# Kernel tuning notes

Measured on AMD Instinct MI355X. Metric: run time of the kernel, lower is better.

## Reference

```python
import jax, jax.numpy as jnp
import numpy as np

N_NODES = 20000
N_EDGES = 320000
D = 256          # out_channels (== in_channels here, so PyG zero-padding is a no-op)
NUM_LAYERS = 5


def setup_inputs() -> dict:
    key = jax.random.key(0)
    ks = jax.random.split(key, 8)
    x = jax.random.normal(ks[0], (N_NODES, D), dtype=jnp.float32)
    src = jax.random.randint(ks[1], (N_EDGES,), 0, N_NODES)
    dst = jax.random.randint(ks[2], (N_EDGES,), 0, N_NODES)
    edge_index = jnp.stack([src, dst]).astype(jnp.int64)
    edge_attr = jax.random.uniform(ks[3], (N_EDGES,), dtype=jnp.float32)
    s = 1.0 / np.sqrt(D)
    # per-layer message transform weights [L, D, D]
    weight = jax.random.uniform(ks[4], (NUM_LAYERS, D, D), minval=-s, maxval=s, dtype=jnp.float32)
    # GRUCell parameters (torch layout: [3*D, D] for W_ih/W_hh, [3*D] biases; gate order r, z, n)
    w_ih = jax.random.uniform(ks[5], (3 * D, D), minval=-s, maxval=s, dtype=jnp.float32)
    w_hh = jax.random.uniform(ks[6], (3 * D, D), minval=-s, maxval=s, dtype=jnp.float32)
    b = jax.random.uniform(ks[7], (2, 3 * D), minval=-s, maxval=s, dtype=jnp.float32)
    return {"x": x, "edge_index": edge_index, "edge_attr": edge_attr,
            "weight": weight, "w_ih": w_ih, "w_hh": w_hh,
            "b_ih": b[0], "b_hh": b[1]}


def gru_cell(m, h, w_ih, w_hh, b_ih, b_hh):
    gi = m @ w_ih.T + b_ih   # [N, 3D]
    gh = h @ w_hh.T + b_hh   # [N, 3D]
    i_r, i_z, i_n = jnp.split(gi, 3, axis=1)
    h_r, h_z, h_n = jnp.split(gh, 3, axis=1)
    r = jax.nn.sigmoid(i_r + h_r)
    z = jax.nn.sigmoid(i_z + h_z)
    n = jnp.tanh(i_n + r * h_n)
    return (1.0 - z) * n + z * h


def reference(x, edge_index, edge_attr, weight, w_ih, w_hh, b_ih, b_hh):
    src = edge_index[0]
    dst = edge_index[1]
    n_nodes = x.shape[0]
    h = x  # in_channels == out_channels, so no zero padding needed
    for i in range(weight.shape[0]):
        m = h @ weight[i]                                  # [N, D] transformed messages
        msgs = m[src] * edge_attr[:, None]                 # gather + edge weighting [E, D]
        agg = jax.ops.segment_sum(msgs, dst, num_segments=n_nodes)  # scatter-add [N, D]
        h = gru_cell(agg, h, w_ih, w_hh, b_ih, b_hh)
    return h
```

## Files before the change

### kernel.cpp

```cpp
#include <hip/hip_runtime.h>
#include <hip/hip_bf16.h>

#define NN 20000
#define NE 320000
#define DD 256

typedef __attribute__((ext_vector_type(8))) short bf16x8;
typedef __attribute__((ext_vector_type(4))) float f32x4;
typedef __attribute__((ext_vector_type(4))) int   int4v;
typedef __attribute__((ext_vector_type(4))) float float4v;

typedef __attribute__((address_space(1))) unsigned int gas_uint;
typedef __attribute__((address_space(3))) unsigned int las_uint;
static __device__ __forceinline__ void gload16(const void* g, void* l) {
    __builtin_amdgcn_global_load_lds((gas_uint*)g, (las_uint*)l, 16, 0, 0);
}

__device__ __forceinline__ unsigned short f2bf(float f) {
    union { float f; unsigned u; } v; v.f = f;
    unsigned r = v.u + 0x7fffu + ((v.u >> 16) & 1u);
    return (unsigned short)(r >> 16);
}
__device__ __forceinline__ float bf2f(unsigned short h) {
    union { unsigned u; float f; } v; v.u = ((unsigned)h) << 16;
    return v.f;
}
__device__ __forceinline__ float fast_sigmoid(float x) {
    return 1.f / (1.f + __expf(-x));
}
__device__ __forceinline__ float fast_tanh(float x) {
    x = fminf(fmaxf(x, -30.f), 30.f);
    float e = __expf(-2.f * x);
    return (1.f - e) / (1.f + e);
}


__global__ void cast_kernel(const float* __restrict__ in, unsigned short* __restrict__ out, int n) {
    int i = (blockIdx.x * blockDim.x + threadIdx.x) * 4;
    if (i >= n) return;
    float4v v = *reinterpret_cast<const float4v*>(in + i);
    uint2 o;
    o.x = (unsigned)f2bf(v.x) | ((unsigned)f2bf(v.y) << 16);
    o.y = (unsigned)f2bf(v.z) | ((unsigned)f2bf(v.w) << 16);
    *reinterpret_cast<uint2*>(out + i) = o;
}

__global__ __launch_bounds__(256) void pgemm_kernel(const unsigned short* __restrict__ A,
                                                    const unsigned short* __restrict__ Bt,
                                                    unsigned short* __restrict__ C) {
    __shared__ __align__(16) unsigned short As[128 * 64];
    __shared__ __align__(16) unsigned short Bs[64 * 64];
    const int t = threadIdx.x;
    const int lane = t & 63;
    const int w = t >> 6;
    const int wr = w >> 1, wc = w & 1;
    const int m0 = blockIdx.y * 128;
    const int n0 = blockIdx.x * 64;

    f32x4 acc[4][2];
    const f32x4 z4 = {0.f, 0.f, 0.f, 0.f};
    for (int i = 0; i < 4; ++i) for (int j = 0; j < 2; ++j) acc[i][j] = z4;

    for (int kt = 0; kt < 4; ++kt) {
        const int k0 = kt * 64;
#pragma unroll
        for (int rnd = 0; rnd < 4; ++rnd) {
            int cb = rnd * 256 + (w << 6);
            int c = cb + lane;
            int row = c >> 3, sl = c & 7;
            int gsl = sl ^ (row & 7);
            gload16(A + (size_t)(m0 + row) * 256 + k0 + gsl * 8, &As[cb * 8]);
        }
#pragma unroll
        for (int rnd = 0; rnd < 2; ++rnd) {
            int cb = rnd * 256 + (w << 6);
            int c = cb + lane;
            int row = c >> 3, sl = c & 7;
            int gsl = sl ^ (row & 7);
            gload16(Bt + (size_t)(n0 + row) * 256 + k0 + gsl * 8, &Bs[cb * 8]);
        }
        __syncthreads();
#pragma unroll
        for (int ks = 0; ks < 2; ++ks) {
            const int slot = ks * 4 + (lane >> 4);
            bf16x8 a[4], b[2];
#pragma unroll
            for (int mi = 0; mi < 4; ++mi) {
                int row = wr * 64 + mi * 16 + (lane & 15);
                a[mi] = *reinterpret_cast<const bf16x8*>(&As[row * 64 + ((slot ^ (row & 7)) << 3)]);
            }
#pragma unroll
            for (int ni = 0; ni < 2; ++ni) {
                int row = wc * 32 + ni * 16 + (lane & 15);
                b[ni] = *reinterpret_cast<const bf16x8*>(&Bs[row * 64 + ((slot ^ (row & 7)) << 3)]);
            }
#pragma unroll
            for (int mi = 0; mi < 4; ++mi)
#pragma unroll
                for (int ni = 0; ni < 2; ++ni)
                    acc[mi][ni] = __builtin_amdgcn_mfma_f32_16x16x32_bf16(a[mi], b[ni], acc[mi][ni], 0, 0, 0);
        }
        __syncthreads();
    }
#pragma unroll
    for (int mi = 0; mi < 4; ++mi)
#pragma unroll
        for (int ni = 0; ni < 2; ++ni)
#pragma unroll
            for (int r = 0; r < 4; ++r) {
                int grow = m0 + wr * 64 + mi * 16 + (lane >> 4) * 4 + r;
                int gcol = n0 + wc * 32 + ni * 16 + (lane & 15);
                C[(size_t)grow * 768 + gcol] = f2bf(acc[mi][ni][r]);
            }
}

__global__ void wc5_kernel(const unsigned short* __restrict__ Pall,
                           const float* __restrict__ whh,
                           unsigned short* __restrict__ Wc5) {
    int id = blockIdx.x * 256 + threadIdx.x;
    int k  = id & 255;
    int t2 = id >> 8;
    int n3 = t2 % 768;
    int t3 = t2 / 768;
    int hf = t3 & 1;
    int l  = t3 >> 1;
    int g3 = (n3 >> 4) % 3;
    int dg = n3 / 48;
    int dc = n3 & 15;
    int d  = dg * 16 + dc;
    int gate_row = g3 * 256 + d;
    unsigned short v;
    if (hf == 0) v = Pall[((size_t)(l * 256 + k)) * 768 + gate_row];
    else         v = f2bf(whh[(size_t)gate_row * 256 + k]);
    Wc5[id] = v;
}


__global__ void hist_kernel(const int* __restrict__ dst, int* __restrict__ deg) {
    int e = blockIdx.x * 256 + threadIdx.x;
    if (e < NE) atomicAdd(&deg[dst[e]], 1);
}

__global__ __launch_bounds__(1024) void scan_kernel(const int* __restrict__ deg, int* __restrict__ base) {
    __shared__ int part[1024];
    const int t = threadIdx.x;
    const int CH = 20;
    int start = t * CH;
    int s = 0;
    for (int i = 0; i < CH; ++i) { int idx = start + i; if (idx < NN) s += deg[idx]; }
    part[t] = s; __syncthreads();
    for (int off = 1; off < 1024; off <<= 1) {
        int v = (t >= off) ? part[t - off] : 0;
        __syncthreads();
        part[t] += v;
        __syncthreads();
    }
    int run = (t == 0) ? 0 : part[t - 1];
    for (int i = 0; i < CH; ++i) {
        int idx = start + i;
        if (idx < NN) { base[idx] = run; run += deg[idx]; }
    }
    if (t == 1023) base[NN] = run;
}

__global__ void fill_kernel(const int* __restrict__ src, const int* __restrict__ dst,
                            const float* __restrict__ attr, const int* __restrict__ base,
                            int* __restrict__ cursor, int* __restrict__ ssrc,
                            float* __restrict__ sattr) {
    int e = blockIdx.x * 256 + threadIdx.x;
    if (e >= NE) return;
    int d = dst[e];
    int pos = base[d] + atomicAdd(&cursor[d], 1);
    ssrc[pos] = src[e];
    sattr[pos] = attr[e];
}

__global__ __launch_bounds__(256) void gather_agg_kernel(const unsigned short* __restrict__ Hbf,
                                                         const int* __restrict__ base,
                                                         const int* __restrict__ ssrc,
                                                         const float* __restrict__ sattr,
                                                         unsigned short* __restrict__ AggBf) {
    int node = blockIdx.x * 4 + (threadIdx.x >> 6);
    if (node >= NN) return;
    int lane = threadIdx.x & 63;
    int q = lane >> 4;
    int ql = lane & 15;
    int b0 = base[node], b1 = base[node + 1];
    float ac[16];
#pragma unroll
    for (int j = 0; j < 16; ++j) ac[j] = 0.f;
    for (int p = b0 + q; p < b1; p += 4) {
        int s = ssrc[p];
        float a = sattr[p];
        const unsigned short* rowp = Hbf + (size_t)s * 256 + ql * 16;
        int4v v0 = *reinterpret_cast<const int4v*>(rowp);
        int4v v1 = *reinterpret_cast<const int4v*>(rowp + 8);
#pragma unroll
        for (int j = 0; j < 4; ++j) {
            unsigned u0 = (unsigned)v0[j];
            ac[2 * j]     += a * bf2f((unsigned short)(u0 & 0xffff));
            ac[2 * j + 1] += a * bf2f((unsigned short)(u0 >> 16));
            unsigned u1 = (unsigned)v1[j];
            ac[8 + 2 * j]     += a * bf2f((unsigned short)(u1 & 0xffff));
            ac[8 + 2 * j + 1] += a * bf2f((unsigned short)(u1 >> 16));
        }
    }
#pragma unroll
    for (int j = 0; j < 16; ++j) {
        ac[j] += __shfl_xor(ac[j], 16);
        ac[j] += __shfl_xor(ac[j], 32);
    }
    if (q == 0) {
        unsigned ou[8];
#pragma unroll
        for (int j = 0; j < 8; ++j)
            ou[j] = (unsigned)f2bf(ac[2 * j]) | ((unsigned)f2bf(ac[2 * j + 1]) << 16);
        unsigned short* op = AggBf + (size_t)node * 256 + ql * 16;
        *reinterpret_cast<int4v*>(op)     = *reinterpret_cast<int4v*>(&ou[0]);
        *reinterpret_cast<int4v*>(op + 8) = *reinterpret_cast<int4v*>(&ou[4]);
    }
}

__global__ __launch_bounds__(1024) void gru5_kernel(const unsigned short* __restrict__ Abf,
                                                    const unsigned short* __restrict__ Hbf,
                                                    const unsigned short* __restrict__ Wc,
                                                    const float* __restrict__ b_ih,
                                                    const float* __restrict__ b_hh,
                                                    const float* __restrict__ x_f32,
                                                    float* __restrict__ h_out,
                                                    unsigned short* __restrict__ Hbf_out,
                                                    int first, int last) {
    __shared__ __align__(16) unsigned short As[128 * 64];
    __shared__ __align__(16) unsigned short Bs[192 * 64];
    const int t = threadIdx.x;
    const int lane = t & 63;
    const int w = t >> 6;
    const int wm = w >> 2, wn = w & 3;
    int b = blockIdx.x;
    int ww = (b & 7) * 79 + (b >> 3);
    const int mt = ww >> 2, dgp = ww & 3;
    const int m0 = mt * 128;

    f32x4 aR[2], aZ[2], aI[2], aH[2];
    const f32x4 z4 = {0.f, 0.f, 0.f, 0.f};
#pragma unroll
    for (int i = 0; i < 2; ++i) { aR[i] = z4; aZ[i] = z4; aI[i] = z4; aH[i] = z4; }

    auto do_half = [&](const unsigned short* __restrict__ aptr,
                       const unsigned short* __restrict__ wcb,
                       f32x4 (&aX)[2]) {
        for (int kq = 0; kq < 4; ++kq) {
            const int ka = kq * 64;
            {
                int cb = (w << 6);
                int c = cb + lane;
                int row = c >> 3, sl = c & 7;
                int gsl = sl ^ (row & 7);
                gload16(aptr + (size_t)(m0 + row) * 256 + ka + gsl * 8, &As[cb * 8]);
            }
            {
                int cb = (w << 6);
                int c = cb + lane;
                int row = c >> 3, sl = c & 7;
                int gsl = sl ^ (row & 7);
                gload16(wcb + (size_t)(dgp * 192 + row) * 256 + ka + gsl * 8, &Bs[cb * 8]);
            }
            if (w < 8) {
                int cb = 1024 + (w << 6);
                int c = cb + lane;
                int row = c >> 3, sl = c & 7;
                int gsl = sl ^ (row & 7);
                gload16(wcb + (size_t)(dgp * 192 + row) * 256 + ka + gsl * 8, &Bs[cb * 8]);
            }
            __syncthreads();
#pragma unroll
            for (int ks = 0; ks < 2; ++ks) {
                const int slot = ks * 4 + (lane >> 4);
                bf16x8 a[2], bfr[3];
#pragma unroll
                for (int mi = 0; mi < 2; ++mi) {
                    int row = wm * 32 + mi * 16 + (lane & 15);
                    a[mi] = *reinterpret_cast<const bf16x8*>(&As[row * 64 + ((slot ^ (row & 7)) << 3)]);
                }
#pragma unroll
                for (int g3 = 0; g3 < 3; ++g3) {
                    int row = wn * 48 + g3 * 16 + (lane & 15);
                    bfr[g3] = *reinterpret_cast<const bf16x8*>(&Bs[row * 64 + ((slot ^ (row & 7)) << 3)]);
                }
#pragma unroll
                for (int mi = 0; mi < 2; ++mi) {
                    aR[mi] = __builtin_amdgcn_mfma_f32_16x16x32_bf16(a[mi], bfr[0], aR[mi], 0, 0, 0);
                    aZ[mi] = __builtin_amdgcn_mfma_f32_16x16x32_bf16(a[mi], bfr[1], aZ[mi], 0, 0, 0);
                    aX[mi] = __builtin_amdgcn_mfma_f32_16x16x32_bf16(a[mi], bfr[2], aX[mi], 0, 0, 0);
                }
            }
            __syncthreads();
        }
    };

    do_half(Abf, Wc, aI);
    do_half(Hbf, Wc + 768 * 256, aH);

    const int d = (dgp * 4 + wn) * 16 + (lane & 15);
    const float bir = b_ih[d],        bhr = b_hh[d];
    const float biz = b_ih[256 + d],  bhz = b_hh[256 + d];
    const float bin_ = b_ih[512 + d], bhn = b_hh[512 + d];
#pragma unroll
    for (int mi = 0; mi < 2; ++mi)
#pragma unroll
        for (int r = 0; r < 4; ++r) {
            int grow = m0 + wm * 32 + mi * 16 + (lane >> 4) * 4 + r;
            if (grow >= NN) continue;
            size_t idx = (size_t)grow * 256 + d;
            float rr = fast_sigmoid(aR[mi][r] + bir + bhr);
            float zz = fast_sigmoid(aZ[mi][r] + biz + bhz);
            float nn = fast_tanh(aI[mi][r] + bin_ + rr * (aH[mi][r] + bhn));
            float hp = first ? x_f32[idx] : bf2f(Hbf[idx]);
            float hv = (1.f - zz) * nn + zz * hp;
            if (last) h_out[idx] = hv;
            Hbf_out[idx] = f2bf(hv);
        }
}


extern "C" void kernel_launch(void* const* d_in, const int* in_sizes, int n_in,
                              void* d_out, int out_size, void* d_ws, size_t ws_size,
                              hipStream_t stream) {
    const float* x     = (const float*)d_in[0];
    const int*   eidx  = (const int*)d_in[1];
    const float* eattr = (const float*)d_in[2];
    const float* W     = (const float*)d_in[3];
    const float* wih   = (const float*)d_in[4];
    const float* whh   = (const float*)d_in[5];
    const float* bih   = (const float*)d_in[6];
    const float* bhh   = (const float*)d_in[7];
    float* out = (float*)d_out;
    const int* esrc = eidx;
    const int* edst = eidx + NE;

    char* p = (char*)d_ws;
    auto alloc = [&](size_t bytes) -> char* {
        char* r = p; p += (bytes + 255) & ~(size_t)255; return r;
    };
    unsigned short* hbfA  = (unsigned short*)alloc((size_t)NN * DD * 2);
    unsigned short* hbfB  = (unsigned short*)alloc((size_t)NN * DD * 2);
    unsigned short* aggbf = (unsigned short*)alloc((size_t)NN * DD * 2);
    unsigned short* wnb   = (unsigned short*)alloc((size_t)5 * DD * DD * 2);
    unsigned short* wihb  = (unsigned short*)alloc((size_t)768 * DD * 2);
    unsigned short* pall  = (unsigned short*)alloc((size_t)1280 * 768 * 2);
    unsigned short* wc5   = (unsigned short*)alloc((size_t)5 * 2 * 768 * 256 * 2);
    int*   deg    = (int*)alloc((size_t)NN * 4);
    int*   basep  = (int*)alloc((size_t)(NN + 1) * 4);
    int*   cursor = (int*)alloc((size_t)NN * 4);
    int*   ssrc   = (int*)alloc((size_t)NE * 4);
    float* sattr  = (float*)alloc((size_t)NE * 4);
    alloc(262144);

    hipMemsetAsync(deg, 0, (size_t)NN * 4, stream);
    hipMemsetAsync(cursor, 0, (size_t)NN * 4, stream);

    cast_kernel<<<320, 256, 0, stream>>>(W, wnb, 5 * DD * DD);
    cast_kernel<<<192, 256, 0, stream>>>(wih, wihb, 768 * DD);
    cast_kernel<<<5000, 256, 0, stream>>>(x, hbfA, NN * DD);
    pgemm_kernel<<<dim3(12, 10), 256, 0, stream>>>(wnb, wihb, pall);
    wc5_kernel<<<7680, 256, 0, stream>>>(pall, whh, wc5);
    hist_kernel<<<1250, 256, 0, stream>>>(edst, deg);
    scan_kernel<<<1, 1024, 0, stream>>>(deg, basep);
    fill_kernel<<<1250, 256, 0, stream>>>(esrc, edst, eattr, basep, cursor, ssrc, sattr);

    unsigned short* hb_cur = hbfA;
    unsigned short* hb_nxt = hbfB;
    for (int l = 0; l < 5; ++l) {
        gather_agg_kernel<<<5000, 256, 0, stream>>>(hb_cur, basep, ssrc, sattr, aggbf);
        gru5_kernel<<<632, 1024, 0, stream>>>(aggbf, hb_cur, wc5 + (size_t)l * 2 * 768 * 256,
                                              bih, bhh, x, out, hb_nxt,
                                              (l == 0) ? 1 : 0, (l == 4) ? 1 : 0);
        unsigned short* tmp = hb_cur; hb_cur = hb_nxt; hb_nxt = tmp;
    }
    (void)in_sizes; (void)n_in; (void)out_size; (void)ws_size;
}
```

Before: 388.4 us.

## Restructure GRU GEMM as single K=512 double-buffered MFMA with concatenated weights

Rebuilds the fused GRU weight matrix as a [1024 x 512] block per layer, holding agg and h weights side by side with zero blocks for the n-gate halves. The GRU kernel then runs one K=512 GEMM with 192x256 tiles, 512 threads, double-buffered LDS staging via global_load_lds, explicit vmcnt waits and barriers, and raised priority around the MFMA issue. This is meant to overlap loads with compute and enlarge per-wave reuse. In exchange it does extra MFMA work on the zero blocks, roughly a third more, and uses more LDS per block.

```diff
diff --git a/kernel.cpp b/kernel.cpp
--- a/kernel.cpp
+++ b/kernel.cpp
@@ -15,6 +15,9 @@
 static __device__ __forceinline__ void gload16(const void* g, void* l) {
     __builtin_amdgcn_global_load_lds((gas_uint*)g, (las_uint*)l, 16, 0, 0);
 }
+
+#define SBAR()   asm volatile("s_barrier" ::: "memory")
+#define WAITV(N) asm volatile("s_waitcnt vmcnt(" #N ")" ::: "memory")
 
 __device__ __forceinline__ unsigned short f2bf(float f) {
     union { float f; unsigned u; } v; v.f = f;
@@ -114,25 +117,30 @@
             }
 }
 
-__global__ void wc5_kernel(const unsigned short* __restrict__ Pall,
+__global__ void wc4_kernel(const unsigned short* __restrict__ Pall,
                            const float* __restrict__ whh,
-                           unsigned short* __restrict__ Wc5) {
+                           unsigned short* __restrict__ Wc45) {
     int id = blockIdx.x * 256 + threadIdx.x;
-    int k  = id & 255;
-    int t2 = id >> 8;
-    int n3 = t2 % 768;
-    int t3 = t2 / 768;
-    int hf = t3 & 1;
-    int l  = t3 >> 1;
-    int g3 = (n3 >> 4) % 3;
-    int dg = n3 / 48;
-    int dc = n3 & 15;
-    int d  = dg * 16 + dc;
-    int gate_row = g3 * 256 + d;
+    int l = id >> 19;
+    int rem = id & 524287;
+    int np = rem >> 9, k = rem & 511;
+    int g = (np >> 4) & 3;
+    int d = ((np >> 6) << 4) | (np & 15);
     unsigned short v;
-    if (hf == 0) v = Pall[((size_t)(l * 256 + k)) * 768 + gate_row];
-    else         v = f2bf(whh[(size_t)gate_row * 256 + k]);
-    Wc5[id] = v;
+    if (k < 256) {
+        if (g == 3) v = 0;
+        else {
+            int gate_row = (g == 2 ? 512 : g * 256) + d;
+            v = Pall[((size_t)(l * 256 + k)) * 768 + gate_row];
+        }
+    } else {
+        if (g == 2) v = 0;
+        else {
+            int gate_row = (g == 3 ? 512 : g * 256) + d;
+            v = f2bf(whh[(size_t)gate_row * 256 + (k - 256)]);
+        }
+    }
+    Wc45[id] = v;
 }
 
 
@@ -221,100 +229,107 @@
     }
 }
 
-__global__ __launch_bounds__(1024) void gru5_kernel(const unsigned short* __restrict__ Abf,
-                                                    const unsigned short* __restrict__ Hbf,
-                                                    const unsigned short* __restrict__ Wc,
-                                                    const float* __restrict__ b_ih,
-                                                    const float* __restrict__ b_hh,
-                                                    const float* __restrict__ x_f32,
-                                                    float* __restrict__ h_out,
-                                                    unsigned short* __restrict__ Hbf_out,
-                                                    int first, int last) {
-    __shared__ __align__(16) unsigned short As[128 * 64];
-    __shared__ __align__(16) unsigned short Bs[192 * 64];
+__global__ __launch_bounds__(512) void gru7_kernel(const unsigned short* __restrict__ Abf,
+                                                   const unsigned short* __restrict__ Hbf,
+                                                   const unsigned short* __restrict__ Wc4,
+                                                   const float* __restrict__ b_ih,
+                                                   const float* __restrict__ b_hh,
+                                                   const float* __restrict__ x_f32,
+                                                   float* __restrict__ h_out,
+                                                   unsigned short* __restrict__ Hbf_out,
+                                                   int first, int last) {
+    __shared__ __align__(16) unsigned short As[2][192 * 64];
+    __shared__ __align__(16) unsigned short Bs[2][256 * 64];
     const int t = threadIdx.x;
     const int lane = t & 63;
     const int w = t >> 6;
     const int wm = w >> 2, wn = w & 3;
     int b = blockIdx.x;
-    int ww = (b & 7) * 79 + (b >> 3);
-    const int mt = ww >> 2, dgp = ww & 3;
-    const int m0 = mt * 128;
-
-    f32x4 aR[2], aZ[2], aI[2], aH[2];
+    int xcd = b & 7, loc = b >> 3;
+    int ww = (xcd < 4 ? xcd * 53 : 4 * 53 + (xcd - 4) * 52) + loc;
+    const int nt = ww & 3, mt = ww >> 2;
+    const int m0 = mt * 192;
+    const int n0 = nt * 256;
+
+    f32x4 acc[6][4];
     const f32x4 z4 = {0.f, 0.f, 0.f, 0.f};
 #pragma unroll
-    for (int i = 0; i < 2; ++i) { aR[i] = z4; aZ[i] = z4; aI[i] = z4; aH[i] = z4; }
-
-    auto do_half = [&](const unsigned short* __restrict__ aptr,
-                       const unsigned short* __restrict__ wcb,
-                       f32x4 (&aX)[2]) {
-        for (int kq = 0; kq < 4; ++kq) {
-            const int ka = kq * 64;
-            {
-                int cb = (w << 6);
-                int c = cb + lane;
-                int row = c >> 3, sl = c & 7;
-                int gsl = sl ^ (row & 7);
-                gload16(aptr + (size_t)(m0 + row) * 256 + ka + gsl * 8, &As[cb * 8]);
-            }
-            {
-                int cb = (w << 6);
-                int c = cb + lane;
-                int row = c >> 3, sl = c & 7;
-                int gsl = sl ^ (row & 7);
-                gload16(wcb + (size_t)(dgp * 192 + row) * 256 + ka + gsl * 8, &Bs[cb * 8]);
-            }
-            if (w < 8) {
-                int cb = 1024 + (w << 6);
-                int c = cb + lane;
-                int row = c >> 3, sl = c & 7;
-                int gsl = sl ^ (row & 7);
-                gload16(wcb + (size_t)(dgp * 192 + row) * 256 + ka + gsl * 8, &Bs[cb * 8]);
-            }
-            __syncthreads();
-#pragma unroll
-            for (int ks = 0; ks < 2; ++ks) {
-                const int slot = ks * 4 + (lane >> 4);
-                bf16x8 a[2], bfr[3];
-#pragma unroll
-                for (int mi = 0; mi < 2; ++mi) {
-                    int row = wm * 32 + mi * 16 + (lane & 15);
-                    a[mi] = *reinterpret_cast<const bf16x8*>(&As[row * 64 + ((slot ^ (row & 7)) << 3)]);
-                }
-#pragma unroll
-                for (int g3 = 0; g3 < 3; ++g3) {
-                    int row = wn * 48 + g3 * 16 + (lane & 15);
-                    bfr[g3] = *reinterpret_cast<const bf16x8*>(&Bs[row * 64 + ((slot ^ (row & 7)) << 3)]);
-                }
-#pragma unroll
-                for (int mi = 0; mi < 2; ++mi) {
-                    aR[mi] = __builtin_amdgcn_mfma_f32_16x16x32_bf16(a[mi], bfr[0], aR[mi], 0, 0, 0);
-                    aZ[mi] = __builtin_amdgcn_mfma_f32_16x16x32_bf16(a[mi], bfr[1], aZ[mi], 0, 0, 0);
-                    aX[mi] = __builtin_amdgcn_mfma_f32_16x16x32_bf16(a[mi], bfr[2], aX[mi], 0, 0, 0);
-                }
-            }
-            __syncthreads();
+    for (int i = 0; i < 6; ++i)
+#pragma unroll
+        for (int j = 0; j < 4; ++j) acc[i][j] = z4;
+
+    auto stage = [&](int buf, int kt) {
+        const unsigned short* aptr = (kt < 4) ? Abf : Hbf;
+        const int ka = (kt & 3) * 64;
+        const int kb = kt * 64;
+#pragma unroll
+        for (int rnd = 0; rnd < 3; ++rnd) {
+            int c = rnd * 512 + t;
+            int row = c >> 3, sl = c & 7;
+            int gsl = sl ^ (row & 7);
+            gload16(aptr + (size_t)(m0 + row) * 256 + ka + gsl * 8, &As[buf][c * 8]);
+        }
+#pragma unroll
+        for (int rnd = 0; rnd < 4; ++rnd) {
+            int c = rnd * 512 + t;
+            int row = c >> 3, sl = c & 7;
+            int gsl = sl ^ (row & 7);
+            gload16(Wc4 + (size_t)(n0 + row) * 512 + kb + gsl * 8, &Bs[buf][c * 8]);
         }
     };
 
-    do_half(Abf, Wc, aI);
-    do_half(Hbf, Wc + 768 * 256, aH);
-
-    const int d = (dgp * 4 + wn) * 16 + (lane & 15);
+    stage(0, 0);
+    for (int kt = 0; kt < 8; ++kt) {
+        const int cur = kt & 1;
+        if (kt < 7) {
+            stage(cur ^ 1, kt + 1);
+            WAITV(7);
+        } else {
+            WAITV(0);
+        }
+        SBAR();
+#pragma unroll
+        for (int ph = 0; ph < 4; ++ph) {
+            const int ks = ph >> 1, mh = ph & 1;
+            const int slot = ks * 4 + (lane >> 4);
+            bf16x8 a[3], bb[4];
+#pragma unroll
+            for (int j = 0; j < 3; ++j) {
+                int arow = wm * 96 + (mh * 3 + j) * 16 + (lane & 15);
+                a[j] = *reinterpret_cast<const bf16x8*>(&As[cur][arow * 64 + ((slot ^ (arow & 7)) << 3)]);
+            }
+#pragma unroll
+            for (int ni = 0; ni < 4; ++ni) {
+                int brow = wn * 64 + ni * 16 + (lane & 15);
+                bb[ni] = *reinterpret_cast<const bf16x8*>(&Bs[cur][brow * 64 + ((slot ^ (brow & 7)) << 3)]);
+            }
+            SBAR();
+            __builtin_amdgcn_s_setprio(1);
+#pragma unroll
+            for (int j = 0; j < 3; ++j)
+#pragma unroll
+                for (int ni = 0; ni < 4; ++ni)
+                    acc[mh * 3 + j][ni] = __builtin_amdgcn_mfma_f32_16x16x32_bf16(a[j], bb[ni], acc[mh * 3 + j][ni], 0, 0, 0);
+            __builtin_amdgcn_s_setprio(0);
+            SBAR();
+        }
+    }
+
+    const int cc = lane & 15;
+    const int d = (nt * 4 + wn) * 16 + cc;
     const float bir = b_ih[d],        bhr = b_hh[d];
     const float biz = b_ih[256 + d],  bhz = b_hh[256 + d];
     const float bin_ = b_ih[512 + d], bhn = b_hh[512 + d];
 #pragma unroll
-    for (int mi = 0; mi < 2; ++mi)
+    for (int mi = 0; mi < 6; ++mi)
 #pragma unroll
         for (int r = 0; r < 4; ++r) {
-            int grow = m0 + wm * 32 + mi * 16 + (lane >> 4) * 4 + r;
+            int grow = m0 + wm * 96 + mi * 16 + (lane >> 4) * 4 + r;
             if (grow >= NN) continue;
             size_t idx = (size_t)grow * 256 + d;
-            float rr = fast_sigmoid(aR[mi][r] + bir + bhr);
-            float zz = fast_sigmoid(aZ[mi][r] + biz + bhz);
-            float nn = fast_tanh(aI[mi][r] + bin_ + rr * (aH[mi][r] + bhn));
+            float rr = fast_sigmoid(acc[mi][0][r] + bir + bhr);
+            float zz = fast_sigmoid(acc[mi][1][r] + biz + bhz);
+            float nn = fast_tanh(acc[mi][2][r] + bin_ + rr * (acc[mi][3][r] + bhn));
             float hp = first ? x_f32[idx] : bf2f(Hbf[idx]);
             float hv = (1.f - zz) * nn + zz * hp;
             if (last) h_out[idx] = hv;
@@ -348,7 +363,7 @@
     unsigned short* wnb   = (unsigned short*)alloc((size_t)5 * DD * DD * 2);
     unsigned short* wihb  = (unsigned short*)alloc((size_t)768 * DD * 2);
     unsigned short* pall  = (unsigned short*)alloc((size_t)1280 * 768 * 2);
-    unsigned short* wc5   = (unsigned short*)alloc((size_t)5 * 2 * 768 * 256 * 2);
+    unsigned short* wc45  = (unsigned short*)alloc((size_t)5 * 1024 * 512 * 2);
     int*   deg    = (int*)alloc((size_t)NN * 4);
     int*   basep  = (int*)alloc((size_t)(NN + 1) * 4);
     int*   cursor = (int*)alloc((size_t)NN * 4);
@@ -363,7 +378,7 @@
     cast_kernel<<<192, 256, 0, stream>>>(wih, wihb, 768 * DD);
     cast_kernel<<<5000, 256, 0, stream>>>(x, hbfA, NN * DD);
     pgemm_kernel<<<dim3(12, 10), 256, 0, stream>>>(wnb, wihb, pall);
-    wc5_kernel<<<7680, 256, 0, stream>>>(pall, whh, wc5);
+    wc4_kernel<<<10240, 256, 0, stream>>>(pall, whh, wc45);
     hist_kernel<<<1250, 256, 0, stream>>>(edst, deg);
     scan_kernel<<<1, 1024, 0, stream>>>(deg, basep);
     fill_kernel<<<1250, 256, 0, stream>>>(esrc, edst, eattr, basep, cursor, ssrc, sattr);
@@ -372,9 +387,9 @@
     unsigned short* hb_nxt = hbfB;
     for (int l = 0; l < 5; ++l) {
         gather_agg_kernel<<<5000, 256, 0, stream>>>(hb_cur, basep, ssrc, sattr, aggbf);
-        gru5_kernel<<<632, 1024, 0, stream>>>(aggbf, hb_cur, wc5 + (size_t)l * 2 * 768 * 256,
-                                              bih, bhh, x, out, hb_nxt,
-                                              (l == 0) ? 1 : 0, (l == 4) ? 1 : 0);
+        gru7_kernel<<<420, 512, 0, stream>>>(aggbf, hb_cur, wc45 + (size_t)l * 1024 * 512,
+                                             bih, bhh, x, out, hb_nxt,
+                                             (l == 0) ? 1 : 0, (l == 4) ? 1 : 0);
         unsigned short* tmp = hb_cur; hb_cur = hb_nxt; hb_nxt = tmp;
     }
     (void)in_sizes; (void)n_in; (void)out_size; (void)ws_size;
```

Measured after the change: 443.8 us. +14.3%, slower.
